# Kernel tuning notes

Hardware: AMD Instinct MI355X
Metric: run time of the kernel (lower is better)

## Reference

```python
import jax, jax.numpy as jnp
import numpy as np

HID = 128          # args.hid
HEADS = 1          # args.head (forced: concat=True and classifier expects 3*hid)
C = HID            # out_channels per head
ND, NPR, NCL = 4096, 20000, 1024
E_DD, E_DP, E_CP = 500_000, 1_000_000, 500_000
B = 8192
SLOPE = 0.2        # GATConv negative_slope default


def _gat(x_src, x_dst, src, dst, W, a_src, a_dst, bias, num_dst,
         edge_attr=None, W_edge=None, a_edge=None):
    # PyG GATConv: shared lin for src/dst (in_channels is int)
    hs = (x_src @ W).reshape(-1, HEADS, C)            # [Ns,H,C]
    hd = (x_dst @ W).reshape(-1, HEADS, C)            # [Nd,H,C]
    e = jnp.sum(hs * a_src, -1)[src] + jnp.sum(hd * a_dst, -1)[dst]  # [E,H]
    if edge_attr is not None:
        ee = (edge_attr @ W_edge).reshape(-1, HEADS, C)
        e = e + jnp.sum(ee * a_edge, -1)
    e = jnp.where(e > 0, e, SLOPE * e)                # leaky_relu
    emax = jax.ops.segment_max(e, dst, num_segments=num_dst)
    ex = jnp.exp(e - emax[dst])
    denom = jax.ops.segment_sum(ex, dst, num_segments=num_dst)
    alpha = ex / (denom[dst] + 1e-16)                 # PyG softmax eps
    out = jax.ops.segment_sum(hs[src] * alpha[:, :, None], dst, num_segments=num_dst)
    return out.reshape(num_dst, HEADS * C) + bias


def _l2n(x):
    return x / jnp.maximum(jnp.linalg.norm(x, axis=1, keepdims=True), 1e-12)


def setup_inputs() -> dict:
    key = jax.random.key(0)
    ks = iter(jax.random.split(key, 48))

    def nrm(shape, s=0.1):
        return jax.random.normal(next(ks), shape, jnp.float32) * s

    inp = {
        'x_drug': jnp.arange(ND, dtype=jnp.int32),
        'x_protein': jnp.arange(NPR, dtype=jnp.int32),
        'x_cell': jnp.arange(NCL, dtype=jnp.int32),
        'ei_dd': jax.random.randint(next(ks), (2, E_DD), 0, ND),
        'edge_attr_dd': jax.random.normal(next(ks), (E_DD, 1), jnp.float32),
        'src_dp': jax.random.randint(next(ks), (E_DP,), 0, NPR),
        'dst_dp': jax.random.randint(next(ks), (E_DP,), 0, ND),
        'src_cp': jax.random.randint(next(ks), (E_CP,), 0, NPR),
        'dst_cp': jax.random.randint(next(ks), (E_CP,), 0, NCL),
        'drug1': jax.random.randint(next(ks), (B,), 0, ND),
        'drug2': jax.random.randint(next(ks), (B,), 0, ND),
        'cell': jax.random.randint(next(ks), (B,), 0, NCL),
        # embedding tables
        'drug_emb': nrm((ND, HID), 1.0),
        'protein_emb': nrm((NPR, HID), 1.0),
        'cell_emb': nrm((NCL, HID), 1.0),
        # GAT d-d (edge_dim=1)
        'W_dd': nrm((HID, HEADS * C)), 'a_src_dd': nrm((HEADS, C)), 'a_dst_dd': nrm((HEADS, C)),
        'bias_dd': jnp.zeros((HEADS * C,), jnp.float32),
        'W_edge_dd': nrm((1, HEADS * C)), 'a_edge_dd': nrm((HEADS, C)),
        # GAT protein->drug
        'W_dp': nrm((HID, HEADS * C)), 'a_src_dp': nrm((HEADS, C)), 'a_dst_dp': nrm((HEADS, C)),
        'bias_dp': jnp.zeros((HEADS * C,), jnp.float32),
        # GAT protein->cell
        'W_cp': nrm((HID, HEADS * C)), 'a_src_cp': nrm((HEADS, C)), 'a_dst_cp': nrm((HEADS, C)),
        'bias_cp': jnp.zeros((HEADS * C,), jnp.float32),
        # classifier: 3h -> 6h -> 2h -> 2
        'W1': nrm((3 * HID, 6 * HID)), 'b1': jnp.zeros((6 * HID,), jnp.float32),
        'W2': nrm((6 * HID, 2 * HID)), 'b2': jnp.zeros((2 * HID,), jnp.float32),
        'W3': nrm((2 * HID, 2)), 'b3': jnp.zeros((2,), jnp.float32),
    }
    return inp


def reference(x_drug, x_protein, x_cell, ei_dd, edge_attr_dd, src_dp, dst_dp,
              src_cp, dst_cp, drug1, drug2, cell, drug_emb, protein_emb, cell_emb,
              W_dd, a_src_dd, a_dst_dd, bias_dd, W_edge_dd, a_edge_dd,
              W_dp, a_src_dp, a_dst_dp, bias_dp,
              W_cp, a_src_cp, a_dst_cp, bias_cp,
              W1, b1, W2, b2, W3, b3):
    h_d = drug_emb[x_drug]
    h_p = protein_emb[x_protein]
    h_c = cell_emb[x_cell]

    # d-d: add self-loops with edge_attr fill_value='mean' (PyG default)
    src, dst = ei_dd[0], ei_dd[1]
    deg = jax.ops.segment_sum(jnp.ones((E_DD,), jnp.float32), dst, num_segments=ND)
    mean_attr = jax.ops.segment_sum(edge_attr_dd, dst, num_segments=ND) / jnp.maximum(deg, 1.0)[:, None]
    loops = jnp.arange(ND, dtype=src.dtype)
    src2 = jnp.concatenate([src, loops])
    dst2 = jnp.concatenate([dst, loops])
    attr2 = jnp.concatenate([edge_attr_dd, mean_attr], 0)

    out_dd = _gat(h_d, h_d, src2, dst2, W_dd, a_src_dd, a_dst_dd, bias_dd, ND,
                  attr2, W_edge_dd, a_edge_dd)
    out_dp = _gat(h_p, h_d, src_dp, dst_dp, W_dp, a_src_dp, a_dst_dp, bias_dp, ND)
    out_cp = _gat(h_p, h_c, src_cp, dst_cp, W_cp, a_src_cp, a_dst_cp, bias_cp, NCL)

    drug = jax.nn.relu(out_dd + out_dp)   # HeteroConv aggr='sum', then F.relu
    cellx = jax.nn.relu(out_cp)

    hid = jnp.concatenate([_l2n(drug[drug1]), _l2n(drug[drug2]), _l2n(cellx[cell])], 1)
    h = jax.nn.relu(hid @ W1 + b1)        # dropout = identity in eval
    h = jax.nn.relu(h @ W2 + b2)
    return h @ W3 + b3
```

## Files before the change

### kernel.cpp

```cpp
#include <hip/hip_runtime.h>
#include <hip/hip_bf16.h>

#define HIDC 128
typedef __hip_bfloat16 bf16;
typedef __attribute__((ext_vector_type(8))) short short8;
typedef __attribute__((ext_vector_type(4))) float floatx4;

#define CHUNK 4096

__device__ __forceinline__ short f2b(float f) {
    unsigned int u = __builtin_bit_cast(unsigned int, f);
    u += 0x7fff + ((u >> 16) & 1);
    return (short)(u >> 16);
}

__global__ void __launch_bounds__(256) r8_prep(
    int* __restrict__ zptr, int zwords, int nzb,
    const float* __restrict__ W_dd, const float* __restrict__ W_dp, const float* __restrict__ W_cp,
    const float* __restrict__ a0, const float* __restrict__ a1, const float* __restrict__ a2,
    const float* __restrict__ a3, const float* __restrict__ a4, const float* __restrict__ a5,
    const float* __restrict__ W_edge, const float* __restrict__ a_edge,
    float* __restrict__ wa, float* __restrict__ c_edge,
    const float* __restrict__ W1, short* __restrict__ Wt1, int nT1,
    const float* __restrict__ W2, short* __restrict__ Wt2)
{
    int b = blockIdx.x;
    int tid = threadIdx.x;
    if (b < nzb) {
        int i = b * 256 + tid;
        if (i < zwords) zptr[i] = 0;
        return;
    }
    b -= nzb;
    if (b < 7) {
        __shared__ float as[HIDC];
        int k = tid;
        if (b < 6) {
            const float* W = (b < 2) ? W_dd : (b < 4) ? W_dp : W_cp;
            const float* a = (b == 0) ? a0 : (b == 1) ? a1 : (b == 2) ? a2 : (b == 3) ? a3 : (b == 4) ? a4 : a5;
            if (k < HIDC) as[k] = a[k];
            __syncthreads();
            if (k < HIDC) {
                float s = 0.f;
#pragma unroll 8
                for (int c = 0; c < HIDC; c++) s = fmaf(W[k * HIDC + c], as[c], s);
                wa[b * HIDC + k] = s;
            }
        } else {
            if (k < HIDC) as[k] = W_edge[k] * a_edge[k];
            __syncthreads();
#pragma unroll
            for (int off = 64; off > 0; off >>= 1) { if (k < off) as[k] += as[k + off]; __syncthreads(); }
            if (k == 0) c_edge[0] = as[0];
        }
        return;
    }
    b -= 7;
    const float* W; short* Wt; int K, N, k0, n0;
    if (b < nT1) { W = W1; Wt = Wt1; K = 384; N = 768; k0 = (b / 24) * 32; n0 = (b % 24) * 32; }
    else { b -= nT1; W = W2; Wt = Wt2; K = 768; N = 256; k0 = (b / 8) * 32; n0 = (b % 8) * 32; }
    __shared__ short T[32 * 34];
    int cc = tid & 31, rr = tid >> 5;
#pragma unroll
    for (int it = 0; it < 4; it++) {
        int r = it * 8 + rr;
        T[r * 34 + cc] = f2b(W[(size_t)(k0 + r) * N + n0 + cc]);
    }
    __syncthreads();
#pragma unroll
    for (int it = 0; it < 4; it++) {
        int r = it * 8 + rr;
        Wt[(size_t)(n0 + r) * K + k0 + cc] = T[cc * 34 + r];
    }
}

__global__ void __launch_bounds__(256) r8_scalars(
    const float* __restrict__ drug_emb, const float* __restrict__ prot_emb, const float* __restrict__ cell_emb,
    const int* __restrict__ x_drug, const int* __restrict__ x_prot, const int* __restrict__ x_cell,
    const float* __restrict__ wa,
    float* __restrict__ ssrc_dd, float* __restrict__ sdst_dd, float* __restrict__ sdst_dp,
    float* __restrict__ ssrc_dp, float* __restrict__ ssrc_cp, float* __restrict__ sdst_cp,
    int nd, int npr, int ncl)
{
    int g = blockIdx.x * 4 + (threadIdx.x >> 6);
    int l = threadIdx.x & 63;
    const float2* wa2 = (const float2*)wa;
    if (g < nd) {
        int id = x_drug[g];
        float2 e = ((const float2*)drug_emb)[(size_t)id * 64 + l];
        float2 w0 = wa2[0 * 64 + l], w1 = wa2[1 * 64 + l], w3 = wa2[3 * 64 + l];
        float p0 = e.x * w0.x + e.y * w0.y;
        float p1 = e.x * w1.x + e.y * w1.y;
        float p2 = e.x * w3.x + e.y * w3.y;
#pragma unroll
        for (int off = 32; off > 0; off >>= 1) {
            p0 += __shfl_xor(p0, off, 64);
            p1 += __shfl_xor(p1, off, 64);
            p2 += __shfl_xor(p2, off, 64);
        }
        if (l == 0) { ssrc_dd[g] = p0; sdst_dd[g] = p1; sdst_dp[g] = p2; }
    } else if (g < nd + npr) {
        int r = g - nd;
        int id = x_prot[r];
        float2 e = ((const float2*)prot_emb)[(size_t)id * 64 + l];
        float2 w2 = wa2[2 * 64 + l], w4 = wa2[4 * 64 + l];
        float p0 = e.x * w2.x + e.y * w2.y;
        float p1 = e.x * w4.x + e.y * w4.y;
#pragma unroll
        for (int off = 32; off > 0; off >>= 1) {
            p0 += __shfl_xor(p0, off, 64);
            p1 += __shfl_xor(p1, off, 64);
        }
        if (l == 0) { ssrc_dp[r] = p0; ssrc_cp[r] = p1; }
    } else if (g < nd + npr + ncl) {
        int r = g - nd - npr;
        int id = x_cell[r];
        float2 e = ((const float2*)cell_emb)[(size_t)id * 64 + l];
        float2 w5 = wa2[5 * 64 + l];
        float p0 = e.x * w5.x + e.y * w5.y;
#pragma unroll
        for (int off = 32; off > 0; off >>= 1) p0 += __shfl_xor(p0, off, 64);
        if (l == 0) sdst_cp[r] = p0;
    }
}

__global__ void __launch_bounds__(128) r8_node_gemm(
    const float* __restrict__ drug_emb, const int* __restrict__ x_drug,
    const float* __restrict__ W_dd, bf16* __restrict__ H_dd, int ndb,
    const float* __restrict__ prot_emb, const int* __restrict__ x_prot,
    const float* __restrict__ W_dp, const float* __restrict__ W_cp,
    bf16* __restrict__ H_dp, bf16* __restrict__ H_cp)
{
    __shared__ int ids[16];
    __shared__ float xs[16 * HIDC];
    int bb = blockIdx.x;
    bool isdrug = bb < ndb;
    int r0 = (isdrug ? bb : bb - ndb) * 16;
    const float* emb = isdrug ? drug_emb : prot_emb;
    const int* idx = isdrug ? x_drug : x_prot;
    int tid = threadIdx.x;
    if (tid < 16) ids[tid] = idx[r0 + tid];
    __syncthreads();
    for (int t = tid; t < 16 * HIDC; t += 128) {
        int r = t >> 7, k = t & 127;
        xs[t] = emb[(size_t)ids[r] * HIDC + k];
    }
    __syncthreads();
    int c = tid;
    if (isdrug) {
        float acc[16];
#pragma unroll
        for (int r = 0; r < 16; r++) acc[r] = 0.f;
        for (int k = 0; k < HIDC; k += 4) {
            float w0 = W_dd[(k + 0) * HIDC + c];
            float w1 = W_dd[(k + 1) * HIDC + c];
            float w2 = W_dd[(k + 2) * HIDC + c];
            float w3 = W_dd[(k + 3) * HIDC + c];
#pragma unroll
            for (int r = 0; r < 16; r++) {
                float4 x = *(const float4*)&xs[r * HIDC + k];
                acc[r] = fmaf(x.x, w0, fmaf(x.y, w1, fmaf(x.z, w2, fmaf(x.w, w3, acc[r]))));
            }
        }
#pragma unroll
        for (int r = 0; r < 16; r++) H_dd[(size_t)(r0 + r) * HIDC + c] = __float2bfloat16(acc[r]);
    } else {
        float accA[16], accB[16];
#pragma unroll
        for (int r = 0; r < 16; r++) { accA[r] = 0.f; accB[r] = 0.f; }
        for (int k = 0; k < HIDC; k += 2) {
            float a0 = W_dp[(k + 0) * HIDC + c];
            float a1 = W_dp[(k + 1) * HIDC + c];
            float b0 = W_cp[(k + 0) * HIDC + c];
            float b1 = W_cp[(k + 1) * HIDC + c];
#pragma unroll
            for (int r = 0; r < 16; r++) {
                float2 x = *(const float2*)&xs[r * HIDC + k];
                accA[r] = fmaf(x.x, a0, fmaf(x.y, a1, accA[r]));
                accB[r] = fmaf(x.x, b0, fmaf(x.y, b1, accB[r]));
            }
        }
#pragma unroll
        for (int r = 0; r < 16; r++) {
            H_dp[(size_t)(r0 + r) * HIDC + c] = __float2bfloat16(accA[r]);
            H_cp[(size_t)(r0 + r) * HIDC + c] = __float2bfloat16(accB[r]);
        }
    }
}

__global__ void __launch_bounds__(256) r8_edge_pass1(
    const int* __restrict__ dst_dd, const float* __restrict__ attr_dd, int E_dd, int nb_dd,
    const int* __restrict__ dst_dp, int E_dp, int nb_dp,
    const int* __restrict__ dst_cp, int E_cp,
    int nd, int ncl,
    int* __restrict__ cnt_dd, float* __restrict__ attr_sum,
    int* __restrict__ cnt_dp, int* __restrict__ cnt_cp,
    int* __restrict__ rank_dd, int* __restrict__ rank_dp, int* __restrict__ rank_cp)
{
    __shared__ int lcnt[4096];
    __shared__ float lattr[4096];
    int bid = blockIdx.x;
    const int* dst; const float* attr = nullptr; int E, e0, bins;
    int* gcnt; int* rank;
    if (bid < nb_dd) {
        dst = dst_dd; attr = attr_dd; E = E_dd; e0 = bid * CHUNK; bins = nd;
        gcnt = cnt_dd; rank = rank_dd;
    } else if (bid < nb_dd + nb_dp) {
        dst = dst_dp; E = E_dp; e0 = (bid - nb_dd) * CHUNK; bins = nd;
        gcnt = cnt_dp; rank = rank_dp;
    } else {
        dst = dst_cp; E = E_cp; e0 = (bid - nb_dd - nb_dp) * CHUNK; bins = ncl;
        gcnt = cnt_cp; rank = rank_cp;
    }
    int tid = threadIdx.x;
    for (int b = tid; b < bins; b += 256) { lcnt[b] = 0; if (attr) lattr[b] = 0.f; }
    __syncthreads();
    int e1 = min(e0 + CHUNK, E);
    for (int i = e0 + tid; i < e1; i += 256) {
        int d = dst[i];
        rank[i] = atomicAdd(&lcnt[d], 1);
        if (attr) atomicAdd(&lattr[d], attr[i]);
    }
    __syncthreads();
    for (int b = tid; b < bins; b += 256) {
        int c = lcnt[b];
        if (c > 0) {
            lcnt[b] = atomicAdd(&gcnt[b], c);
            if (attr) atomicAdd(&attr_sum[b], lattr[b]);
        }
    }
    __syncthreads();
    for (int i = e0 + tid; i < e1; i += 256) {
        rank[i] += lcnt[dst[i]];
    }
}

__global__ void __launch_bounds__(1024) r8_exscan3(
    const int* __restrict__ in0, int* __restrict__ out0, int n0,
    const int* __restrict__ in1, int* __restrict__ out1, int n1,
    const int* __restrict__ in2, int* __restrict__ out2, int n2)
{
    const int* in; int* out; int n; int inc;
    if (blockIdx.x == 0)      { in = in0; out = out0; n = n0; inc = 1; }
    else if (blockIdx.x == 1) { in = in1; out = out1; n = n1; inc = 0; }
    else                      { in = in2; out = out2; n = n2; inc = 0; }
    __shared__ int buf[1024];
    __shared__ int carry;
    int tid = threadIdx.x;
    if (tid == 0) carry = 0;
    __syncthreads();
    for (int base = 0; base < n; base += 1024) {
        int i = base + tid;
        int v = (i < n) ? (in[i] + inc) : 0;
        buf[tid] = v; __syncthreads();
        for (int off = 1; off < 1024; off <<= 1) {
            int t = (tid >= off) ? buf[tid - off] : 0;
            __syncthreads();
            buf[tid] += t;
            __syncthreads();
        }
        int c0 = carry;
        int incl = buf[tid];
        if (i < n) out[i] = c0 + incl - v;
        __syncthreads();
        if (tid == 1023) carry = c0 + buf[1023];
        __syncthreads();
    }
    if (tid == 0) out[n] = carry;
}

__global__ void r8_scatter(
    const int* __restrict__ ei_dd, const float* __restrict__ attr_dd, int E_dd, int nd,
    const int* __restrict__ src_dp, const int* __restrict__ dst_dp, int E_dp,
    const int* __restrict__ src_cp, const int* __restrict__ dst_cp, int E_cp,
    const int* __restrict__ rank_dd, const int* __restrict__ rank_dp, const int* __restrict__ rank_cp,
    const int* __restrict__ deg_dd, const float* __restrict__ attr_sum,
    const float* __restrict__ c_edge_ptr,
    const float* __restrict__ ssrc_dd, const float* __restrict__ sdst_dd,
    const float* __restrict__ ssrc_dp, const float* __restrict__ sdst_dp,
    const float* __restrict__ ssrc_cp, const float* __restrict__ sdst_cp,
    const int* __restrict__ rs_dd, const int* __restrict__ rs_dp, const int* __restrict__ rs_cp,
    int2* __restrict__ csr_dd, int2* __restrict__ csr_dp, int2* __restrict__ csr_cp)
{
    int i = blockIdx.x * 256 + threadIdx.x;
    if (i < E_dd) {
        int s = ei_dd[i], d = ei_dd[E_dd + i];
        float ev = ssrc_dd[s] + sdst_dd[d] + attr_dd[i] * c_edge_ptr[0];
        ev = (ev > 0.f) ? ev : 0.2f * ev;
        csr_dd[rs_dd[d] + rank_dd[i]] = make_int2(s, __float_as_int(ev));
        return;
    }
    i -= E_dd;
    if (i < nd) {
        int d = i;
        int dg = deg_dd[d];
        float mean = attr_sum[d] / fmaxf((float)dg, 1.0f);
        float ev = ssrc_dd[d] + sdst_dd[d] + mean * c_edge_ptr[0];
        ev = (ev > 0.f) ? ev : 0.2f * ev;
        csr_dd[rs_dd[d] + dg] = make_int2(d, __float_as_int(ev));
        return;
    }
    i -= nd;
    if (i < E_dp) {
        int d = dst_dp[i], s = src_dp[i];
        float ev = ssrc_dp[s] + sdst_dp[d];
        ev = (ev > 0.f) ? ev : 0.2f * ev;
        csr_dp[rs_dp[d] + rank_dp[i]] = make_int2(s, __float_as_int(ev));
        return;
    }
    i -= E_dp;
    if (i < E_cp) {
        int d = dst_cp[i], s = src_cp[i];
        float ev = ssrc_cp[s] + sdst_cp[d];
        ev = (ev > 0.f) ? ev : 0.2f * ev;
        csr_cp[rs_cp[d] + rank_cp[i]] = make_int2(s, __float_as_int(ev));
    }
}

__global__ void __launch_bounds__(64) r8_agg3(
    const int* __restrict__ rs_dd, const int2* __restrict__ csr_dd, const uint* __restrict__ Hdd,
    float* __restrict__ agg_dd, int nd,
    const int* __restrict__ rs_dp, const int2* __restrict__ csr_dp, const uint* __restrict__ Hdp,
    float* __restrict__ agg_dp,
    const int* __restrict__ rs_cp, const int2* __restrict__ csr_cp, const uint* __restrict__ Hcp,
    float* __restrict__ agg_cp)
{
    int b = blockIdx.x;
    const int* rs; const int2* csr; const uint* H2; float* out; int row;
    if (b < nd)          { rs = rs_dd; csr = csr_dd; H2 = Hdd; out = agg_dd; row = b; }
    else if (b < 2 * nd) { rs = rs_dp; csr = csr_dp; H2 = Hdp; out = agg_dp; row = b - nd; }
    else                 { rs = rs_cp; csr = csr_cp; H2 = Hcp; out = agg_cp; row = b - 2 * nd; }
    int t = threadIdx.x;
    int s = rs[row], e = rs[row + 1];
    float sum = 0.f;
    for (int i = s + t; i < e; i += 64) sum += __expf(__int_as_float(csr[i].y));
#pragma unroll
    for (int off = 32; off > 0; off >>= 1) sum += __shfl_xor(sum, off, 64);
    float inv = 1.f / (sum + 1e-16f);

    __shared__ float se[64];
    __shared__ int ss[64];
    float accx = 0.f, accy = 0.f;
    int base = s;
    for (; base + 64 <= e; base += 64) {
        int2 c = csr[base + t];
        se[t] = __expf(__int_as_float(c.y));
        ss[t] = c.x;
        __syncthreads();
#pragma unroll 8
        for (int j = 0; j < 64; j++) {
            uint u = H2[(size_t)ss[j] * 64 + t];
            float w = se[j];
            accx = fmaf(w, __uint_as_float(u << 16), accx);
            accy = fmaf(w, __uint_as_float(u & 0xffff0000u), accy);
        }
        __syncthreads();
    }
    if (base < e) {
        int i = base + t;
        if (i < e) {
            int2 c = csr[i];
            se[t] = __expf(__int_as_float(c.y));
            ss[t] = c.x;
        }
        __syncthreads();
        int lim = e - base;
        for (int j = 0; j < lim; j++) {
            uint u = H2[(size_t)ss[j] * 64 + t];
            float w = se[j];
            accx = fmaf(w, __uint_as_float(u << 16), accx);
            accy = fmaf(w, __uint_as_float(u & 0xffff0000u), accy);
        }
        __syncthreads();
    }
    float2 o; o.x = accx * inv; o.y = accy * inv;
    ((float2*)out)[(size_t)row * 64 + t] = o;
}

__global__ void __launch_bounds__(128) r8_fuse(
    const float* __restrict__ agg_dd, const float* __restrict__ bias_dd,
    const float* __restrict__ agg_dp, const float* __restrict__ bias_dp,
    float* __restrict__ drugN, int nd,
    const float* __restrict__ agg_cp, const float* __restrict__ bias_cp,
    float* __restrict__ cellN)
{
    int b = blockIdx.x, c = threadIdx.x;
    float v;
    float* outN;
    int d;
    if (b < nd) {
        d = b;
        v = agg_dd[(size_t)d * HIDC + c] + bias_dd[c] + agg_dp[(size_t)d * HIDC + c] + bias_dp[c];
        outN = drugN;
    } else {
        d = b - nd;
        v = agg_cp[(size_t)d * HIDC + c] + bias_cp[c];
        outN = cellN;
    }
    v = fmaxf(v, 0.f);
    __shared__ float red[HIDC];
    red[c] = v * v; __syncthreads();
#pragma unroll
    for (int off = 64; off > 0; off >>= 1) { if (c < off) red[c] += red[c + off]; __syncthreads(); }
    float nrm = fmaxf(sqrtf(red[0]), 1e-12f);
    outN[(size_t)d * HIDC + c] = v / nrm;
}

__global__ void __launch_bounds__(128) r8_gather_hid(
    const float* __restrict__ drugN, const float* __restrict__ cellN,
    const int* __restrict__ d1, const int* __restrict__ d2, const int* __restrict__ ce,
    short* __restrict__ hid)
{
    int b = blockIdx.x, c = threadIdx.x;
    hid[(size_t)b * 384 + c]       = f2b(drugN[(size_t)d1[b] * HIDC + c]);
    hid[(size_t)b * 384 + 128 + c] = f2b(drugN[(size_t)d2[b] * HIDC + c]);
    hid[(size_t)b * 384 + 256 + c] = f2b(cellN[(size_t)ce[b] * HIDC + c]);
}

template <int NB, int OUT_BF16>
__global__ void __launch_bounds__(256) r8_mgemm(
    const short* __restrict__ X, const short* __restrict__ Wt, const float* __restrict__ bias,
    void* __restrict__ Y, int M, int K, int N)
{
    constexpr int BN = NB * 16;
    __shared__ short As[128 * 40];
    __shared__ short Bs[BN * 40];
    int m0 = blockIdx.x * 128, n0 = blockIdx.y * BN;
    int tid = threadIdx.x;
    int w = tid >> 6, lane = tid & 63;
    int q = lane >> 4, t = lane & 15;
    int sr = tid >> 1, sc = tid & 1;

    floatx4 acc[2][NB];
#pragma unroll
    for (int i = 0; i < 2; i++)
#pragma unroll
        for (int c = 0; c < NB; c++) acc[i][c] = (floatx4){0.f, 0.f, 0.f, 0.f};

    for (int kt = 0; kt < K; kt += 32) {
        {
            const uint4* ga = (const uint4*)(X + (size_t)(m0 + sr) * K + kt + sc * 16);
            uint4 a0 = ga[0], a1 = ga[1];
            *(uint4*)&As[sr * 40 + sc * 16]     = a0;
            *(uint4*)&As[sr * 40 + sc * 16 + 8] = a1;
        }
        for (int tt = tid; tt < BN * 2; tt += 256) {
            int r = tt >> 1, h = tt & 1;
            const uint4* gb = (const uint4*)(Wt + (size_t)(n0 + r) * K + kt + h * 16);
            uint4 b0 = gb[0], b1 = gb[1];
            *(uint4*)&Bs[r * 40 + h * 16]     = b0;
            *(uint4*)&Bs[r * 40 + h * 16 + 8] = b1;
        }
        __syncthreads();
        short8 af[2], bf[NB];
#pragma unroll
        for (int i = 0; i < 2; i++)
            af[i] = *(const short8*)&As[(w * 32 + i * 16 + t) * 40 + q * 8];
#pragma unroll
        for (int c = 0; c < NB; c++)
            bf[c] = *(const short8*)&Bs[(c * 16 + t) * 40 + q * 8];
#pragma unroll
        for (int i = 0; i < 2; i++)
#pragma unroll
            for (int c = 0; c < NB; c++)
                acc[i][c] = __builtin_amdgcn_mfma_f32_16x16x32_bf16(af[i], bf[c], acc[i][c], 0, 0, 0);
        __syncthreads();
    }

    float bv[NB];
#pragma unroll
    for (int c = 0; c < NB; c++) bv[c] = bias[n0 + c * 16 + t];
#pragma unroll
    for (int i = 0; i < 2; i++) {
#pragma unroll
        for (int c = 0; c < NB; c++) {
#pragma unroll
            for (int ii = 0; ii < 4; ii++) {
                int m_g = m0 + w * 32 + i * 16 + q * 4 + ii;
                int n_g = n0 + c * 16 + t;
                float v = acc[i][c][ii] + bv[c];
                v = fmaxf(v, 0.f);
                if (OUT_BF16) ((short*)Y)[(size_t)m_g * N + n_g] = f2b(v);
                else          ((float*)Y)[(size_t)m_g * N + n_g] = v;
            }
        }
    }
}

__global__ void __launch_bounds__(256) r8_final(
    const float* __restrict__ h2, const float* __restrict__ W3, const float* __restrict__ b3,
    float* __restrict__ out)
{
    int row = blockIdx.x * 4 + (threadIdx.x >> 6);
    int lane = threadIdx.x & 63;
    float a0 = 0.f, a1 = 0.f;
    for (int k = lane; k < 256; k += 64) {
        float h = h2[(size_t)row * 256 + k];
        a0 = fmaf(h, W3[k * 2 + 0], a0);
        a1 = fmaf(h, W3[k * 2 + 1], a1);
    }
#pragma unroll
    for (int off = 32; off > 0; off >>= 1) {
        a0 += __shfl_down(a0, off, 64);
        a1 += __shfl_down(a1, off, 64);
    }
    if (lane == 0) {
        out[row * 2 + 0] = a0 + b3[0];
        out[row * 2 + 1] = a1 + b3[1];
    }
}

extern "C" void kernel_launch(void* const* d_in, const int* in_sizes, int n_in,
                              void* d_out, int out_size, void* d_ws, size_t ws_size,
                              hipStream_t stream)
{
    const int* x_drug      = (const int*)d_in[0];
    const int* x_protein   = (const int*)d_in[1];
    const int* x_cell      = (const int*)d_in[2];
    const int* ei_dd       = (const int*)d_in[3];
    const float* attr_dd   = (const float*)d_in[4];
    const int* src_dp      = (const int*)d_in[5];
    const int* dst_dp      = (const int*)d_in[6];
    const int* src_cp      = (const int*)d_in[7];
    const int* dst_cp      = (const int*)d_in[8];
    const int* drug1       = (const int*)d_in[9];
    const int* drug2       = (const int*)d_in[10];
    const int* cellb       = (const int*)d_in[11];
    const float* drug_emb  = (const float*)d_in[12];
    const float* protein_emb = (const float*)d_in[13];
    const float* cell_emb  = (const float*)d_in[14];
    const float* W_dd      = (const float*)d_in[15];
    const float* a_src_dd  = (const float*)d_in[16];
    const float* a_dst_dd  = (const float*)d_in[17];
    const float* bias_dd   = (const float*)d_in[18];
    const float* W_edge_dd = (const float*)d_in[19];
    const float* a_edge_dd = (const float*)d_in[20];
    const float* W_dp      = (const float*)d_in[21];
    const float* a_src_dp  = (const float*)d_in[22];
    const float* a_dst_dp  = (const float*)d_in[23];
    const float* bias_dp   = (const float*)d_in[24];
    const float* W_cp      = (const float*)d_in[25];
    const float* a_src_cp  = (const float*)d_in[26];
    const float* a_dst_cp  = (const float*)d_in[27];
    const float* bias_cp   = (const float*)d_in[28];
    const float* W1        = (const float*)d_in[29];
    const float* b1        = (const float*)d_in[30];
    const float* W2        = (const float*)d_in[31];
    const float* b2        = (const float*)d_in[32];
    const float* W3        = (const float*)d_in[33];
    const float* b3        = (const float*)d_in[34];

    const int ND  = in_sizes[0];
    const int NPR = in_sizes[1];
    const int NCL = in_sizes[2];
    const int E_DD = in_sizes[4];
    const int E_DP = in_sizes[5];
    const int E_CP = in_sizes[7];
    const int B    = in_sizes[9];
    const int E_DD2 = E_DD + ND;

    char* p = (char*)d_ws;
    auto carve = [&](size_t bytes) -> char* {
        char* r = p;
        p += (bytes + 255) & ~(size_t)255;
        return r;
    };
    char* zstart = p;
    int*   cnt_dd   = (int*)  carve((size_t)ND * 4);
    float* attr_sum = (float*)carve((size_t)ND * 4);
    int*   cnt_dp   = (int*)  carve((size_t)ND * 4);
    int*   cnt_cp   = (int*)  carve((size_t)NCL * 4);
    size_t zbytes = (size_t)(p - zstart);
    int*   rs_dd    = (int*)  carve((size_t)(ND + 1) * 4);
    int*   rs_dp    = (int*)  carve((size_t)(ND + 1) * 4);
    int*   rs_cp    = (int*)  carve((size_t)(NCL + 1) * 4);
    float* c_edge   = (float*)carve(256);
    float* wa       = (float*)carve(6 * HIDC * 4);
    bf16*  H_dd     = (bf16*) carve((size_t)ND * HIDC * 2);
    bf16*  H_dp     = (bf16*) carve((size_t)NPR * HIDC * 2);
    bf16*  H_cp     = (bf16*) carve((size_t)NPR * HIDC * 2);
    float* ssrc_dd  = (float*)carve((size_t)ND * 4);
    float* sdst_dd  = (float*)carve((size_t)ND * 4);
    float* ssrc_dp  = (float*)carve((size_t)NPR * 4);
    float* sdst_dp  = (float*)carve((size_t)ND * 4);
    float* ssrc_cp  = (float*)carve((size_t)NPR * 4);
    float* sdst_cp  = (float*)carve((size_t)NCL * 4);
    int*   rank_dd  = (int*)  carve((size_t)E_DD * 4);
    int*   rank_dp  = (int*)  carve((size_t)E_DP * 4);
    int*   rank_cp  = (int*)  carve((size_t)E_CP * 4);
    int2*  csr_dd   = (int2*) carve((size_t)E_DD2 * 8);
    int2*  csr_dp   = (int2*) carve((size_t)E_DP * 8);
    int2*  csr_cp   = (int2*) carve((size_t)E_CP * 8);
    float* agg_dd   = (float*)carve((size_t)ND * HIDC * 4);
    float* agg_dp   = (float*)carve((size_t)ND * HIDC * 4);
    float* agg_cp   = (float*)carve((size_t)NCL * HIDC * 4);
    float* drugN    = (float*)carve((size_t)ND * HIDC * 4);
    float* cellN    = (float*)carve((size_t)NCL * HIDC * 4);
    short* hidb     = (short*)carve((size_t)B * 384 * 2);
    short* h1b      = (short*)carve((size_t)B * 768 * 2);
    float* h2       = (float*)carve((size_t)B * 256 * 4);
    short* Wt1      = (short*)carve((size_t)384 * 768 * 2);
    short* Wt2      = (short*)carve((size_t)768 * 256 * 2);

    auto cdiv = [](int a, int b) { return (a + b - 1) / b; };

    int zwords = (int)(zbytes / 4);
    int nzb = cdiv(zwords, 256);
    int nT1 = (384 / 32) * (768 / 32);
    int nT2 = (768 / 32) * (256 / 32);
    r8_prep<<<nzb + 7 + nT1 + nT2, 256, 0, stream>>>(
        (int*)zstart, zwords, nzb,
        W_dd, W_dp, W_cp, a_src_dd, a_dst_dd, a_src_dp, a_dst_dp, a_src_cp, a_dst_cp,
        W_edge_dd, a_edge_dd, wa, c_edge, W1, Wt1, nT1, W2, Wt2);

    r8_node_gemm<<<ND / 16 + NPR / 16, 128, 0, stream>>>(
        drug_emb, x_drug, W_dd, H_dd, ND / 16,
        protein_emb, x_protein, W_dp, W_cp, H_dp, H_cp);
    r8_scalars<<<(ND + NPR + NCL) / 4, 256, 0, stream>>>(
        drug_emb, protein_emb, cell_emb, x_drug, x_protein, x_cell, wa,
        ssrc_dd, sdst_dd, sdst_dp, ssrc_dp, ssrc_cp, sdst_cp, ND, NPR, NCL);

    int nb_dd = cdiv(E_DD, CHUNK), nb_dp = cdiv(E_DP, CHUNK), nb_cp = cdiv(E_CP, CHUNK);
    r8_edge_pass1<<<nb_dd + nb_dp + nb_cp, 256, 0, stream>>>(
        ei_dd + E_DD, attr_dd, E_DD, nb_dd,
        dst_dp, E_DP, nb_dp,
        dst_cp, E_CP,
        ND, NCL,
        cnt_dd, attr_sum, cnt_dp, cnt_cp, rank_dd, rank_dp, rank_cp);
    r8_exscan3<<<3, 1024, 0, stream>>>(cnt_dd, rs_dd, ND, cnt_dp, rs_dp, ND, cnt_cp, rs_cp, NCL);
    r8_scatter<<<cdiv(E_DD + ND + E_DP + E_CP, 256), 256, 0, stream>>>(
        ei_dd, attr_dd, E_DD, ND, src_dp, dst_dp, E_DP, src_cp, dst_cp, E_CP,
        rank_dd, rank_dp, rank_cp, cnt_dd, attr_sum, c_edge,
        ssrc_dd, sdst_dd, ssrc_dp, sdst_dp, ssrc_cp, sdst_cp,
        rs_dd, rs_dp, rs_cp, csr_dd, csr_dp, csr_cp);

    r8_agg3<<<ND + ND + NCL, 64, 0, stream>>>(
        rs_dd, csr_dd, (const uint*)H_dd, agg_dd, ND,
        rs_dp, csr_dp, (const uint*)H_dp, agg_dp,
        rs_cp, csr_cp, (const uint*)H_cp, agg_cp);

    r8_fuse<<<ND + NCL, 128, 0, stream>>>(agg_dd, bias_dd, agg_dp, bias_dp, drugN, ND,
                                          agg_cp, bias_cp, cellN);

    r8_gather_hid<<<B, 128, 0, stream>>>(drugN, cellN, drug1, drug2, cellb, hidb);
    {
        dim3 g1(B / 128, 768 / 128);
        r8_mgemm<8, 1><<<g1, 256, 0, stream>>>(hidb, Wt1, b1, (void*)h1b, B, 384, 768);
        dim3 g2(B / 128, 256 / 64);
        r8_mgemm<4, 0><<<g2, 256, 0, stream>>>(h1b, Wt2, b2, (void*)h2, B, 768, 256);
    }
    r8_final<<<B / 4, 256, 0, stream>>>(h2, W3, b3, (float*)d_out);
}
```

Before: 346.4 us.

## Pack CSR entries into 32-bit (src<<16 | bf16 exp weight) and split aggregation per half-row

Scatter now computes exp of the edge score once and stores it as bf16 packed with a 16-bit source index in one uint, halving CSR storage and traffic. The aggregation kernel reads the packed word directly, with no exp per pass. Each row is now split across two blocks, each covering half of the columns, with two 32-lane groups interleaving edges and combining via shuffle. This adds parallelism and cuts CSR bytes, but gives up the max-subtraction in softmax and relies on bf16 weight precision and source index below 65536. Each edge also gathers narrower column slices.

```diff
diff --git a/kernel.cpp b/kernel.cpp
--- a/kernel.cpp
+++ b/kernel.cpp
@@ -14,7 +14,12 @@
     return (short)(u >> 16);
 }
 
-__global__ void __launch_bounds__(256) r8_prep(
+__device__ __forceinline__ uint packe(int s, float ev) {
+    float w = __expf(ev);
+    return ((uint)s << 16) | (uint)(unsigned short)f2b(w);
+}
+
+__global__ void __launch_bounds__(256) r10_prep(
     int* __restrict__ zptr, int zwords, int nzb,
     const float* __restrict__ W_dd, const float* __restrict__ W_dp, const float* __restrict__ W_cp,
     const float* __restrict__ a0, const float* __restrict__ a1, const float* __restrict__ a2,
@@ -74,7 +79,7 @@
     }
 }
 
-__global__ void __launch_bounds__(256) r8_scalars(
+__global__ void __launch_bounds__(256) r10_scalars(
     const float* __restrict__ drug_emb, const float* __restrict__ prot_emb, const float* __restrict__ cell_emb,
     const int* __restrict__ x_drug, const int* __restrict__ x_prot, const int* __restrict__ x_cell,
     const float* __restrict__ wa,
@@ -124,7 +129,7 @@
     }
 }
 
-__global__ void __launch_bounds__(128) r8_node_gemm(
+__global__ void __launch_bounds__(128) r10_node_gemm(
     const float* __restrict__ drug_emb, const int* __restrict__ x_drug,
     const float* __restrict__ W_dd, bf16* __restrict__ H_dd, int ndb,
     const float* __restrict__ prot_emb, const int* __restrict__ x_prot,
@@ -188,7 +193,7 @@
     }
 }
 
-__global__ void __launch_bounds__(256) r8_edge_pass1(
+__global__ void __launch_bounds__(256) r10_edge_pass1(
     const int* __restrict__ dst_dd, const float* __restrict__ attr_dd, int E_dd, int nb_dd,
     const int* __restrict__ dst_dp, int E_dp, int nb_dp,
     const int* __restrict__ dst_cp, int E_cp,
@@ -235,7 +240,7 @@
     }
 }
 
-__global__ void __launch_bounds__(1024) r8_exscan3(
+__global__ void __launch_bounds__(1024) r10_exscan3(
     const int* __restrict__ in0, int* __restrict__ out0, int n0,
     const int* __restrict__ in1, int* __restrict__ out1, int n1,
     const int* __restrict__ in2, int* __restrict__ out2, int n2)
@@ -269,7 +274,7 @@
     if (tid == 0) out[n] = carry;
 }
 
-__global__ void r8_scatter(
+__global__ void r10_scatter(
     const int* __restrict__ ei_dd, const float* __restrict__ attr_dd, int E_dd, int nd,
     const int* __restrict__ src_dp, const int* __restrict__ dst_dp, int E_dp,
     const int* __restrict__ src_cp, const int* __restrict__ dst_cp, int E_cp,
@@ -280,14 +285,14 @@
     const float* __restrict__ ssrc_dp, const float* __restrict__ sdst_dp,
     const float* __restrict__ ssrc_cp, const float* __restrict__ sdst_cp,
     const int* __restrict__ rs_dd, const int* __restrict__ rs_dp, const int* __restrict__ rs_cp,
-    int2* __restrict__ csr_dd, int2* __restrict__ csr_dp, int2* __restrict__ csr_cp)
+    uint* __restrict__ csr_dd, uint* __restrict__ csr_dp, uint* __restrict__ csr_cp)
 {
     int i = blockIdx.x * 256 + threadIdx.x;
     if (i < E_dd) {
         int s = ei_dd[i], d = ei_dd[E_dd + i];
         float ev = ssrc_dd[s] + sdst_dd[d] + attr_dd[i] * c_edge_ptr[0];
         ev = (ev > 0.f) ? ev : 0.2f * ev;
-        csr_dd[rs_dd[d] + rank_dd[i]] = make_int2(s, __float_as_int(ev));
+        csr_dd[rs_dd[d] + rank_dd[i]] = packe(s, ev);
         return;
     }
     i -= E_dd;
@@ -297,7 +302,7 @@
         float mean = attr_sum[d] / fmaxf((float)dg, 1.0f);
         float ev = ssrc_dd[d] + sdst_dd[d] + mean * c_edge_ptr[0];
         ev = (ev > 0.f) ? ev : 0.2f * ev;
-        csr_dd[rs_dd[d] + dg] = make_int2(d, __float_as_int(ev));
+        csr_dd[rs_dd[d] + dg] = packe(d, ev);
         return;
     }
     i -= nd;
@@ -305,7 +310,7 @@
         int d = dst_dp[i], s = src_dp[i];
         float ev = ssrc_dp[s] + sdst_dp[d];
         ev = (ev > 0.f) ? ev : 0.2f * ev;
-        csr_dp[rs_dp[d] + rank_dp[i]] = make_int2(s, __float_as_int(ev));
+        csr_dp[rs_dp[d] + rank_dp[i]] = packe(s, ev);
         return;
     }
     i -= E_dp;
@@ -313,71 +318,66 @@
         int d = dst_cp[i], s = src_cp[i];
         float ev = ssrc_cp[s] + sdst_cp[d];
         ev = (ev > 0.f) ? ev : 0.2f * ev;
-        csr_cp[rs_cp[d] + rank_cp[i]] = make_int2(s, __float_as_int(ev));
-    }
-}
-
-__global__ void __launch_bounds__(64) r8_agg3(
-    const int* __restrict__ rs_dd, const int2* __restrict__ csr_dd, const uint* __restrict__ Hdd,
+        csr_cp[rs_cp[d] + rank_cp[i]] = packe(s, ev);
+    }
+}
+
+__global__ void __launch_bounds__(64) r10_agg3(
+    const int* __restrict__ rs_dd, const uint* __restrict__ csr_dd, const uint* __restrict__ Hdd,
     float* __restrict__ agg_dd, int nd,
-    const int* __restrict__ rs_dp, const int2* __restrict__ csr_dp, const uint* __restrict__ Hdp,
+    const int* __restrict__ rs_dp, const uint* __restrict__ csr_dp, const uint* __restrict__ Hdp,
     float* __restrict__ agg_dp,
-    const int* __restrict__ rs_cp, const int2* __restrict__ csr_cp, const uint* __restrict__ Hcp,
-    float* __restrict__ agg_cp)
+    const int* __restrict__ rs_cp, const uint* __restrict__ csr_cp, const uint* __restrict__ Hcp,
+    float* __restrict__ agg_cp, int R)
 {
     int b = blockIdx.x;
-    const int* rs; const int2* csr; const uint* H2; float* out; int row;
-    if (b < nd)          { rs = rs_dd; csr = csr_dd; H2 = Hdd; out = agg_dd; row = b; }
-    else if (b < 2 * nd) { rs = rs_dp; csr = csr_dp; H2 = Hdp; out = agg_dp; row = b - nd; }
-    else                 { rs = rs_cp; csr = csr_cp; H2 = Hcp; out = agg_cp; row = b - 2 * nd; }
+    int slot = b & 7;
+    int half = slot >> 2;
+    int row_g = (b >> 3) * 4 + (slot & 3);
+    if (row_g >= R) return;
+    const int* rs; const uint* csr; const uint* H2; float* out; int row;
+    if (row_g < nd)          { rs = rs_dd; csr = csr_dd; H2 = Hdd; out = agg_dd; row = row_g; }
+    else if (row_g < 2 * nd) { rs = rs_dp; csr = csr_dp; H2 = Hdp; out = agg_dp; row = row_g - nd; }
+    else                     { rs = rs_cp; csr = csr_cp; H2 = Hcp; out = agg_cp; row = row_g - 2 * nd; }
     int t = threadIdx.x;
+    int c = t & 31, g = t >> 5;
     int s = rs[row], e = rs[row + 1];
+
     float sum = 0.f;
-    for (int i = s + t; i < e; i += 64) sum += __expf(__int_as_float(csr[i].y));
+    for (int i = s + t; i < e; i += 64) sum += __uint_as_float((csr[i] & 0xffffu) << 16);
 #pragma unroll
     for (int off = 32; off > 0; off >>= 1) sum += __shfl_xor(sum, off, 64);
     float inv = 1.f / (sum + 1e-16f);
 
     __shared__ float se[64];
     __shared__ int ss[64];
+    const uint* Hh = H2 + half * 32 + c;
     float accx = 0.f, accy = 0.f;
-    int base = s;
-    for (; base + 64 <= e; base += 64) {
-        int2 c = csr[base + t];
-        se[t] = __expf(__int_as_float(c.y));
-        ss[t] = c.x;
+    for (int base = s; base < e; base += 64) {
+        int lim = min(64, e - base);
+        if (t < lim) {
+            uint pk = csr[base + t];
+            se[t] = __uint_as_float((pk & 0xffffu) << 16);
+            ss[t] = (int)(pk >> 16);
+        }
         __syncthreads();
-#pragma unroll 8
-        for (int j = 0; j < 64; j++) {
-            uint u = H2[(size_t)ss[j] * 64 + t];
+        for (int j = g; j < lim; j += 2) {
+            uint u = Hh[(size_t)ss[j] * 64];
             float w = se[j];
             accx = fmaf(w, __uint_as_float(u << 16), accx);
             accy = fmaf(w, __uint_as_float(u & 0xffff0000u), accy);
         }
         __syncthreads();
     }
-    if (base < e) {
-        int i = base + t;
-        if (i < e) {
-            int2 c = csr[i];
-            se[t] = __expf(__int_as_float(c.y));
-            ss[t] = c.x;
-        }
-        __syncthreads();
-        int lim = e - base;
-        for (int j = 0; j < lim; j++) {
-            uint u = H2[(size_t)ss[j] * 64 + t];
-            float w = se[j];
-            accx = fmaf(w, __uint_as_float(u << 16), accx);
-            accy = fmaf(w, __uint_as_float(u & 0xffff0000u), accy);
-        }
-        __syncthreads();
-    }
-    float2 o; o.x = accx * inv; o.y = accy * inv;
-    ((float2*)out)[(size_t)row * 64 + t] = o;
-}
-
-__global__ void __launch_bounds__(128) r8_fuse(
+    accx += __shfl_xor(accx, 32, 64);
+    accy += __shfl_xor(accy, 32, 64);
+    if (t < 32) {
+        float2 o; o.x = accx * inv; o.y = accy * inv;
+        ((float2*)out)[(size_t)row * 64 + half * 32 + c] = o;
+    }
+}
+
+__global__ void __launch_bounds__(128) r10_fuse(
     const float* __restrict__ agg_dd, const float* __restrict__ bias_dd,
     const float* __restrict__ agg_dp, const float* __restrict__ bias_dp,
     float* __restrict__ drugN, int nd,
@@ -406,7 +406,7 @@
     outN[(size_t)d * HIDC + c] = v / nrm;
 }
 
-__global__ void __launch_bounds__(128) r8_gather_hid(
+__global__ void __launch_bounds__(128) r10_gather_hid(
     const float* __restrict__ drugN, const float* __restrict__ cellN,
     const int* __restrict__ d1, const int* __restrict__ d2, const int* __restrict__ ce,
     short* __restrict__ hid)
@@ -418,7 +418,7 @@
 }
 
 template <int NB, int OUT_BF16>
-__global__ void __launch_bounds__(256) r8_mgemm(
+__global__ void __launch_bounds__(256) r10_mgemm(
     const short* __restrict__ X, const short* __restrict__ Wt, const float* __restrict__ bias,
     void* __restrict__ Y, int M, int K, int N)
 {
@@ -487,7 +487,7 @@
     }
 }
 
-__global__ void __launch_bounds__(256) r8_final(
+__global__ void __launch_bounds__(256) r10_final(
     const float* __restrict__ h2, const float* __restrict__ W3, const float* __restrict__ b3,
     float* __restrict__ out)
 {
@@ -588,9 +588,9 @@
     int*   rank_dd  = (int*)  carve((size_t)E_DD * 4);
     int*   rank_dp  = (int*)  carve((size_t)E_DP * 4);
     int*   rank_cp  = (int*)  carve((size_t)E_CP * 4);
-    int2*  csr_dd   = (int2*) carve((size_t)E_DD2 * 8);
-    int2*  csr_dp   = (int2*) carve((size_t)E_DP * 8);
-    int2*  csr_cp   = (int2*) carve((size_t)E_CP * 8);
+    uint*  csr_dd   = (uint*) carve((size_t)E_DD2 * 4);
+    uint*  csr_dp   = (uint*) carve((size_t)E_DP * 4);
+    uint*  csr_cp   = (uint*) carve((size_t)E_CP * 4);
     float* agg_dd   = (float*)carve((size_t)ND * HIDC * 4);
     float* agg_dp   = (float*)carve((size_t)ND * HIDC * 4);
     float* agg_cp   = (float*)carve((size_t)NCL * HIDC * 4);
@@ -608,46 +608,50 @@
     int nzb = cdiv(zwords, 256);
     int nT1 = (384 / 32) * (768 / 32);
     int nT2 = (768 / 32) * (256 / 32);
-    r8_prep<<<nzb + 7 + nT1 + nT2, 256, 0, stream>>>(
+    r10_prep<<<nzb + 7 + nT1 + nT2, 256, 0, stream>>>(
         (int*)zstart, zwords, nzb,
         W_dd, W_dp, W_cp, a_src_dd, a_dst_dd, a_src_dp, a_dst_dp, a_src_cp, a_dst_cp,
         W_edge_dd, a_edge_dd, wa, c_edge, W1, Wt1, nT1, W2, Wt2);
 
-    r8_node_gemm<<<ND / 16 + NPR / 16, 128, 0, stream>>>(
+    r10_node_gemm<<<ND / 16 + NPR / 16, 128, 0, stream>>>(
         drug_emb, x_drug, W_dd, H_dd, ND / 16,
         protein_emb, x_protein, W_dp, W_cp, H_dp, H_cp);
-    r8_scalars<<<(ND + NPR + NCL) / 4, 256, 0, stream>>>(
+    r10_scalars<<<(ND + NPR + NCL) / 4, 256, 0, stream>>>(
         drug_emb, protein_emb, cell_emb, x_drug, x_protein, x_cell, wa,
         ssrc_dd, sdst_dd, sdst_dp, ssrc_dp, ssrc_cp, sdst_cp, ND, NPR, NCL);
 
     int nb_dd = cdiv(E_DD, CHUNK), nb_dp = cdiv(E_DP, CHUNK), nb_cp = cdiv(E_CP, CHUNK);
-    r8_edge_pass1<<<nb_dd + nb_dp + nb_cp, 256, 0, stream>>>(
+    r10_edge_pass1<<<nb_dd + nb_dp + nb_cp, 256, 0, stream>>>(
         ei_dd + E_DD, attr_dd, E_DD, nb_dd,
         dst_dp, E_DP, nb_dp,
         dst_cp, E_CP,
         ND, NCL,
         cnt_dd, attr_sum, cnt_dp, cnt_cp, rank_dd, rank_dp, rank_cp);
-    r8_exscan3<<<3, 1024, 0, stream>>>(cnt_dd, rs_dd, ND, cnt_dp, rs_dp, ND, cnt_cp, rs_cp, NCL);
-    r8_scatter<<<cdiv(E_DD + ND + E_DP + E_CP, 256), 256, 0, stream>>>(
+    r10_exscan3<<<3, 1024, 0, stream>>>(cnt_dd, rs_dd, ND, cnt_dp, rs_dp, ND, cnt_cp, rs_cp, NCL);
+    r10_scatter<<<cdiv(E_DD + ND + E_DP + E_CP, 256), 256, 0, stream>>>(
         ei_dd, attr_dd, E_DD, ND, src_dp, dst_dp, E_DP, src_cp, dst_cp, E_CP,
         rank_dd, rank_dp, rank_cp, cnt_dd, attr_sum, c_edge,
         ssrc_dd, sdst_dd, ssrc_dp, sdst_dp, ssrc_cp, sdst_cp,
         rs_dd, rs_dp, rs_cp, csr_dd, csr_dp, csr_cp);
 
-    r8_agg3<<<ND + ND + NCL, 64, 0, stream>>>(
-        rs_dd, csr_dd, (const uint*)H_dd, agg_dd, ND,
-        rs_dp, csr_dp, (const uint*)H_dp, agg_dp,
-        rs_cp, csr_cp, (const uint*)H_cp, agg_cp);
-
-    r8_fuse<<<ND + NCL, 128, 0, stream>>>(agg_dd, bias_dd, agg_dp, bias_dp, drugN, ND,
-                                          agg_cp, bias_cp, cellN);
-
-    r8_gather_hid<<<B, 128, 0, stream>>>(drugN, cellN, drug1, drug2, cellb, hidb);
+    {
+        int R = 2 * ND + NCL;
+        int G = cdiv(R, 4) * 8;
+        r10_agg3<<<G, 64, 0, stream>>>(
+            rs_dd, csr_dd, (const uint*)H_dd, agg_dd, ND,
+            rs_dp, csr_dp, (const uint*)H_dp, agg_dp,
+            rs_cp, csr_cp, (const uint*)H_cp, agg_cp, R);
+    }
+
+    r10_fuse<<<ND + NCL, 128, 0, stream>>>(agg_dd, bias_dd, agg_dp, bias_dp, drugN, ND,
+                                           agg_cp, bias_cp, cellN);
+
+    r10_gather_hid<<<B, 128, 0, stream>>>(drugN, cellN, drug1, drug2, cellb, hidb);
     {
         dim3 g1(B / 128, 768 / 128);
-        r8_mgemm<8, 1><<<g1, 256, 0, stream>>>(hidb, Wt1, b1, (void*)h1b, B, 384, 768);
+        r10_mgemm<8, 1><<<g1, 256, 0, stream>>>(hidb, Wt1, b1, (void*)h1b, B, 384, 768);
         dim3 g2(B / 128, 256 / 64);
-        r8_mgemm<4, 0><<<g2, 256, 0, stream>>>(h1b, Wt2, b2, (void*)h2, B, 768, 256);
-    }
-    r8_final<<<B / 4, 256, 0, stream>>>(h2, W3, b3, (float*)d_out);
-}
+        r10_mgemm<4, 0><<<g2, 256, 0, stream>>>(h1b, Wt2, b2, (void*)h2, B, 768, 256);
+    }
+    r10_final<<<B / 4, 256, 0, stream>>>(h2, W3, b3, (float*)d_out);
+}
```

Result: slower. 408.1 us (+17.8%).
